# Optimization experiments

Hardware: AMD Instinct MI355X
Metric: run time of the kernel (lower is better)

The kernel has to match this reference:

```python
import jax, jax.numpy as jnp
import numpy as np

B, N, DIN, DOUT, T, R, H = 4, 384, 128, 128, 4, 4, 8
DK = DOUT // H
SQRT_DK = float(np.sqrt(DK))


def setup_inputs() -> dict:
    key = jax.random.key(0)
    k = jax.random.split(key, 12)
    node_features = jax.random.normal(k[0], (B, N, DIN), jnp.float32)
    nt = jax.random.uniform(k[1], (B, N, T), dtype=jnp.float32)
    node_types_soft = nt / nt.sum(-1, keepdims=True)  # soft type distribution
    adj_matrix_soft = jax.random.uniform(k[2], (B, N, N), dtype=jnp.float32)
    et = jax.random.uniform(k[3], (B, N, N, R), dtype=jnp.float32)
    edge_types_soft = et / et.sum(-1, keepdims=True)  # soft relation distribution
    s = 0.05  # ~xavier scale for 128x128
    return dict(
        node_features=node_features,
        node_types_soft=node_types_soft,
        adj_matrix_soft=adj_matrix_soft,
        edge_types_soft=edge_types_soft,
        kw=jax.random.normal(k[4], (T, DIN, DOUT), jnp.float32) * s,
        kb=jnp.zeros((T, DOUT), jnp.float32),
        qw=jax.random.normal(k[5], (T, DIN, DOUT), jnp.float32) * s,
        qb=jnp.zeros((T, DOUT), jnp.float32),
        vw=jax.random.normal(k[6], (T, DIN, DOUT), jnp.float32) * s,
        vb=jnp.zeros((T, DOUT), jnp.float32),
        aw=jax.random.normal(k[7], (T, DOUT, DOUT), jnp.float32) * s,
        ab=jnp.zeros((T, DOUT), jnp.float32),
        norm_w=jnp.ones((T, DOUT), jnp.float32),
        norm_b=jnp.zeros((T, DOUT), jnp.float32),
        rel_pri=jnp.ones((R, H), jnp.float32),
        rel_att=jax.random.normal(k[8], (R, H, DK, DK), jnp.float32) * 0.1,
        rel_msg=jax.random.normal(k[9], (R, H, DK, DK), jnp.float32) * 0.1,
        skip=jnp.ones((T,), jnp.float32),
    )


def _forward(node_features, node_types_soft, adj_matrix_soft, edge_types_soft,
             kw, kb, qw, qb, vw, vb, aw, ab, norm_w, norm_b,
             rel_pri, rel_att, rel_msg, skip):
    Bq, Nn, _ = node_features.shape
    nt = node_types_soft
    # per-type Q/K/V projections: [B,N,T,H,DK]
    q = (jnp.einsum('bni,tid->bntd', node_features, qw) + qb).reshape(Bq, Nn, T, H, DK)
    kk = (jnp.einsum('bni,tid->bntd', node_features, kw) + kb).reshape(Bq, Nn, T, H, DK)
    v = (jnp.einsum('bni,tid->bntd', node_features, vw) + vb).reshape(Bq, Nn, T, H, DK)

    res_att = jnp.zeros((Bq, Nn, Nn, H), node_features.dtype)
    res_msg = jnp.zeros((Bq, Nn, Nn, H, DK), node_features.dtype)
    for r in range(R):  # small fixed relation count; types/heads fully vectorized
        kr = jnp.einsum('bjshe,hed->bjshd', kk, rel_att[r])
        vr = jnp.einsum('bjshe,hed->bjshd', v, rel_msg[r])
        # fold target-type mask (applied at node j in the original) into k: [B,N,Tt,Ts,H,DK]
        krt = kr[:, :, None] * nt[:, :, :, None, None, None]
        # P[b,i,j,s,h] = sum_{t,d} q[b,i,t,h,d] * nt[b,j,t] * kr[b,j,s,h,d], scaled
        P = jnp.einsum('bithd,bjtshd->bijsh', q, krt) * (rel_pri[r] / SQRT_DK)
        mask = edge_types_soft[..., r] * adj_matrix_soft  # [B,N,N]
        res_att = res_att + jnp.einsum('bijsh,bis->bijh', P, nt) * mask[..., None]
        res_msg = res_msg + jnp.einsum('bijsh,bis,bjshd->bijhd', P, nt, vr) * mask[..., None, None]

    att_sum = res_att.sum(axis=1, keepdims=True)
    safe = jnp.where(att_sum > 1e-6, att_sum, jnp.ones_like(att_sum))
    attw = (res_att / safe) * (att_sum > 1e-6).astype(res_att.dtype)
    agg = jnp.einsum('btsh,btshd->bthd', attw, res_msg).reshape(Bq, Nn, DOUT)

    trans = jnp.einsum('bnd,tdo->bnto', agg, aw) + ab
    trans = jax.nn.gelu(trans, approximate=False)  # dropout = identity at eval
    alpha = jax.nn.sigmoid(skip)[None, None, :, None]
    # in_dim == out_dim -> identity skip projection
    res = trans * alpha + node_features[:, :, None, :] * (1.0 - alpha)
    mean = res.mean(-1, keepdims=True)
    var = res.var(-1, keepdims=True)
    res = (res - mean) / jnp.sqrt(var + 1e-5) * norm_w + norm_b
    return (res * nt[..., None]).sum(axis=2)  # [B,N,DOUT]


def reference(node_features, node_types_soft, adj_matrix_soft, edge_types_soft,
              kw, kb, qw, qb, vw, vb, aw, ab, norm_w, norm_b,
              rel_pri, rel_att, rel_msg, skip):
    return _forward(node_features, node_types_soft, adj_matrix_soft, edge_types_soft,
                    kw, kb, qw, qb, vw, vb, aw, ab, norm_w, norm_b,
                    rel_pri, rel_att, rel_msg, skip)
```

## Files before the change

### kernel.cpp

```cpp
#include <hip/hip_runtime.h>
#include <math.h>

#define Bq 4
#define Nn 384
#define NB 1536
#define TT 4
#define RR 4
#define HH 8
#define DKk 16
#define APART 12288

typedef __attribute__((ext_vector_type(8))) short short8;
typedef __attribute__((ext_vector_type(4))) float f32x4;

__device__ __forceinline__ unsigned short f2bf(float f) {
  unsigned u = __float_as_uint(f);
  u += 0x7FFFu + ((u >> 16) & 1u);
  return (unsigned short)(u >> 16);
}

__device__ __forceinline__ void ld16(const float* __restrict__ p, float* o) {
  const float4* p4 = reinterpret_cast<const float4*>(p);
  float4 a = p4[0], b = p4[1], c = p4[2], d = p4[3];
  o[0]=a.x; o[1]=a.y; o[2]=a.z; o[3]=a.w;
  o[4]=b.x; o[5]=b.y; o[6]=b.z; o[7]=b.w;
  o[8]=c.x; o[9]=c.y; o[10]=c.z; o[11]=c.w;
  o[12]=d.x; o[13]=d.y; o[14]=d.z; o[15]=d.w;
}

__device__ __forceinline__ void bar_lds() {
  asm volatile("s_waitcnt lgkmcnt(0)" ::: "memory");
  __builtin_amdgcn_s_barrier();
}


__global__ __launch_bounds__(256) void k1a_qkv(
    const float* __restrict__ nf,
    const float* __restrict__ qw, const float* __restrict__ qb,
    const float* __restrict__ kw, const float* __restrict__ kb,
    const float* __restrict__ vw, const float* __restrict__ vb,
    float* __restrict__ q_ws, float* __restrict__ kv_k, float* __restrict__ kv_v)
{
  __shared__ float A_s[32][72];
  __shared__ float W_s[32][132];
  int mt = blockIdx.x, t = blockIdx.y, z = blockIdx.z;
  const float* W    = (z == 0) ? qw : ((z == 1) ? kw : vw);
  const float* bias = (z == 0) ? qb : ((z == 1) ? kb : vb);
  int tid = threadIdx.x;
  int colq = (tid & 31)*4, n8 = (tid >> 5)*8;
  float acc[8][4];
#pragma unroll
  for (int u = 0; u < 8; ++u)
#pragma unroll
    for (int c = 0; c < 4; ++c) acc[u][c] = 0.f;

  for (int kc = 0; kc < 4; ++kc) {
    __syncthreads();
    {
      int kk = tid & 31, nb0 = tid >> 5;
#pragma unroll
      for (int u = 0; u < 8; ++u)
        A_s[kk][nb0 + u*8] = nf[(size_t)(mt*64 + nb0 + u*8)*128 + kc*32 + kk];
#pragma unroll
      for (int u = 0; u < 4; ++u) {
        int idx = u*256 + tid;
        int wk = idx >> 5, c4 = (idx & 31)*4;
        *(float4*)&W_s[wk][c4] = *(const float4*)&W[(size_t)(t*128 + kc*32 + wk)*128 + c4];
      }
    }
    __syncthreads();
#pragma unroll
    for (int k = 0; k < 32; ++k) {
      float4 w4 = *(float4*)&W_s[k][colq];
      float a0[8];
      *(float4*)&a0[0] = *(float4*)&A_s[k][n8];
      *(float4*)&a0[4] = *(float4*)&A_s[k][n8 + 4];
#pragma unroll
      for (int u = 0; u < 8; ++u) {
        acc[u][0] += a0[u]*w4.x; acc[u][1] += a0[u]*w4.y;
        acc[u][2] += a0[u]*w4.z; acc[u][3] += a0[u]*w4.w;
      }
    }
  }
  float4 bv = *(const float4*)&bias[t*128 + colq];
#pragma unroll
  for (int u = 0; u < 8; ++u) {
    int node = mt*64 + n8 + u;
    float4 o;
    o.x = acc[u][0] + bv.x; o.y = acc[u][1] + bv.y;
    o.z = acc[u][2] + bv.z; o.w = acc[u][3] + bv.w;
    if (z == 0) {
      int h = colq >> 4, d = colq & 15;
      *(float4*)&q_ws[((size_t)h*NB + node)*64 + t*16 + d] = o;
    } else {
      float* dst = (z == 1) ? kv_k : kv_v;
      *(float4*)&dst[(size_t)node*512 + t*128 + colq] = o;
    }
  }
}

__global__ __launch_bounds__(256) void k1b_rel(
    const float* __restrict__ kv_k, const float* __restrict__ kv_v,
    const float* __restrict__ rel_att, const float* __restrict__ rel_msg,
    float* __restrict__ kr_ws, float* __restrict__ vr_ws,
    float* __restrict__ agg)
{
  __shared__ float ra_s[4][16][16];
  __shared__ float rm_s[4][16][16];
  __shared__ float k_s[16][4][17];
  __shared__ float v_s[16][4][17];
  int nb = blockIdx.x, h = blockIdx.y;
  int n0 = nb*16;
  int tid = threadIdx.x;
  agg[(size_t)(n0 + (tid >> 4))*128 + h*16 + (tid & 15)] = 0.f;
#pragma unroll
  for (int u0 = 0; u0 < 4; ++u0) {
    int u = u0*256 + tid;
    int r = u >> 8, e = (u >> 4) & 15, d = u & 15;
    ra_s[r][e][d] = rel_att[((size_t)(r*8 + h)*16 + e)*16 + d];
    rm_s[r][e][d] = rel_msg[((size_t)(r*8 + h)*16 + e)*16 + d];
    int nl = u >> 6, s = (u >> 4) & 3, e2 = u & 15;
    k_s[nl][s][e2] = kv_k[(size_t)(n0 + nl)*512 + s*128 + h*16 + e2];
    v_s[nl][s][e2] = kv_v[(size_t)(n0 + nl)*512 + s*128 + h*16 + e2];
  }
  __syncthreads();
  int nl = tid >> 4, dq = tid & 15;
  size_t obase = ((size_t)h*NB + n0 + nl)*256;
#pragma unroll
  for (int r = 0; r < 4; ++r)
#pragma unroll
    for (int s = 0; s < 4; ++s) {
      float aK = 0.f, aV = 0.f;
#pragma unroll
      for (int e = 0; e < 16; ++e) {
        aK += k_s[nl][s][e] * ra_s[r][e][dq];
        aV += v_s[nl][s][e] * rm_s[r][e][dq];
      }
      kr_ws[obase + r*64 + s*16 + dq] = aK;
      vr_ws[obase + r*64 + s*16 + dq] = aV;
    }
}

__global__ __launch_bounds__(256,2) void k2_att(
    const float* __restrict__ nt, const float* __restrict__ adj,
    const float* __restrict__ ets, const float* __restrict__ rel_pri,
    const float* __restrict__ q_ws, const float* __restrict__ kr_ws,
    float* __restrict__ res_att, float* __restrict__ att_part)
{
  __shared__ float q_s[16*68];
  __shared__ float kr_s[32*260];
  __shared__ float ntj_s[32*4];
  int bx = blockIdx.x, h = blockIdx.y, b = blockIdx.z;
  int it = bx >> 1, jh = bx & 1;
  int i0 = it*16;
  int tid = threadIdx.x;
  int j_l = tid>>3, ig = (tid>>1)&3, dh = tid&1;
  {
    int i = tid>>4, f = (tid&15)*4;
    float4 qv = *(const float4*)&q_ws[((size_t)(h*NB) + b*Nn + i0 + i)*64 + f];
    *(float4*)&q_s[i*68 + f] = qv;
  }
  float ntiv[4][4];
#pragma unroll
  for (int il = 0; il < 4; ++il) {
    float4 v = *(const float4*)&nt[(size_t)(b*Nn + i0 + ig*4 + il)*TT];
    ntiv[il][0]=v.x; ntiv[il][1]=v.y; ntiv[il][2]=v.z; ntiv[il][3]=v.w;
  }
  float crr[4];
#pragma unroll
  for (int r = 0; r < 4; ++r) crr[r] = rel_pri[r*HH+h]*0.25f;

  for (int jc = jh*6; jc < jh*6 + 6; ++jc) {
    __syncthreads();
    {
      int js = tid>>3, gb = tid&7;
      const float* src = &kr_ws[((size_t)(h*NB) + b*Nn + jc*32 + js)*256];
      float* dst = &kr_s[js*260];
#pragma unroll
      for (int gl = 0; gl < 8; ++gl) {
        int g = gl*8 + gb;
        float4 v = *(const float4*)&src[g*4];
        int r = g>>4, s = (g>>2)&3, qd = g&3;
        int gd = (qd>>1)*32 + r*8 + s*2 + (qd&1);
        *(float4*)&dst[gd*4] = v;
      }
      if (tid < 128) ntj_s[tid] = nt[(size_t)(b*Nn + jc*32 + (tid>>2))*TT + (tid&3)];
    }
    __syncthreads();
    int j = jc*32 + j_l;
    float nt0 = ntj_s[j_l*4+0], nt1 = ntj_s[j_l*4+1];
    float nt2 = ntj_s[j_l*4+2], nt3 = ntj_s[j_l*4+3];
    float qn[4][8];
#pragma unroll
    for (int il = 0; il < 4; ++il) {
      const float* qb2 = &q_s[(ig*4 + il)*68 + dh*8];
      float4 a0 = *(const float4*)&qb2[0],  a1 = *(const float4*)&qb2[4];
      float4 b0 = *(const float4*)&qb2[16], b1 = *(const float4*)&qb2[20];
      float4 c0 = *(const float4*)&qb2[32], c1 = *(const float4*)&qb2[36];
      float4 d0v = *(const float4*)&qb2[48], d1v = *(const float4*)&qb2[52];
      qn[il][0] = a0.x*nt0 + b0.x*nt1 + c0.x*nt2 + d0v.x*nt3;
      qn[il][1] = a0.y*nt0 + b0.y*nt1 + c0.y*nt2 + d0v.y*nt3;
      qn[il][2] = a0.z*nt0 + b0.z*nt1 + c0.z*nt2 + d0v.z*nt3;
      qn[il][3] = a0.w*nt0 + b0.w*nt1 + c0.w*nt2 + d0v.w*nt3;
      qn[il][4] = a1.x*nt0 + b1.x*nt1 + c1.x*nt2 + d1v.x*nt3;
      qn[il][5] = a1.y*nt0 + b1.y*nt1 + c1.y*nt2 + d1v.y*nt3;
      qn[il][6] = a1.z*nt0 + b1.z*nt1 + c1.z*nt2 + d1v.z*nt3;
      qn[il][7] = a1.w*nt0 + b1.w*nt1 + c1.w*nt2 + d1v.w*nt3;
    }
    float mar[4][4];
#pragma unroll
    for (int il = 0; il < 4; ++il) {
      int i = i0 + ig*4 + il;
      float a = adj[((size_t)b*Nn + i)*Nn + j];
      float4 e4 = *(const float4*)&ets[(((size_t)b*Nn + i)*Nn + j)*RR];
      mar[il][0]=e4.x*a; mar[il][1]=e4.y*a; mar[il][2]=e4.z*a; mar[il][3]=e4.w*a;
    }
    float acc[4] = {0.f,0.f,0.f,0.f};
    const float* kbp = &kr_s[j_l*260 + dh*128];
#pragma unroll
    for (int r = 0; r < 4; ++r) {
      float mr0 = mar[0][r]*crr[r], mr1 = mar[1][r]*crr[r];
      float mr2 = mar[2][r]*crr[r], mr3 = mar[3][r]*crr[r];
#pragma unroll
      for (int s = 0; s < 4; ++s) {
        float kk[8];
        *(float4*)&kk[0] = *(const float4*)&kbp[r*32 + s*8];
        *(float4*)&kk[4] = *(const float4*)&kbp[r*32 + s*8 + 4];
        float d0=0,d1=0,d2=0,d3=0;
#pragma unroll
        for (int dp = 0; dp < 8; ++dp) {
          d0 += qn[0][dp]*kk[dp]; d1 += qn[1][dp]*kk[dp];
          d2 += qn[2][dp]*kk[dp]; d3 += qn[3][dp]*kk[dp];
        }
        acc[0] += mr0*ntiv[0][s]*d0;
        acc[1] += mr1*ntiv[1][s]*d1;
        acc[2] += mr2*ntiv[2][s]*d2;
        acc[3] += mr3*ntiv[3][s]*d3;
      }
    }
#pragma unroll
    for (int il = 0; il < 4; ++il)
      acc[il] += __shfl_xor(acc[il], 1);
    if (dh == 0) {
#pragma unroll
      for (int il = 0; il < 4; ++il)
        res_att[((size_t)(b*HH + h)*Nn + i0 + ig*4 + il)*Nn + j] = acc[il];
    }
    float v = acc[0] + acc[1] + acc[2] + acc[3];
    v += __shfl_xor(v, 2);
    v += __shfl_xor(v, 4);
    if ((tid & 7) == 0)
      att_part[(size_t)it*APART + (size_t)(b*HH + h)*Nn + j] = v;
  }
}

__global__ __launch_bounds__(256) void kc_agg(
    const float* __restrict__ nt, const float* __restrict__ adj,
    const float* __restrict__ ets, const float* __restrict__ rel_pri,
    const float* __restrict__ q_ws, const float* __restrict__ kr_ws,
    const float* __restrict__ vr_ws, const float* __restrict__ res_att,
    const float* __restrict__ att_part, float* __restrict__ agg)
{
  __shared__ __align__(16) unsigned short B_lds[4][64*72];
  __shared__ __align__(16) unsigned short vr_lds[64*72];
  __shared__ __align__(16) unsigned short Z_lds[4][16*72];
  __shared__ float ntj_s[256];
  __shared__ float inv_s[64];
  int it = blockIdx.x, jc = blockIdx.y, bh = blockIdx.z;
  int b = bh >> 3, h = bh & 7;
  int tid = threadIdx.x, w = tid >> 6, l = tid & 63;
  int j0 = jc*64;
  int ib = it*64 + w*16;
  int irow = ib + (l & 15);
  int iz = ib + ((l >> 4) << 2);
  int lq = (l >> 4) * 8;
  ntj_s[tid] = nt[(size_t)(b*Nn + j0 + (tid>>2))*4 + (tid&3)];
  if (tid < 64) {
    float s = 0.f;
#pragma unroll
    for (int p = 0; p < 24; ++p)
      s += att_part[(size_t)p*APART + (size_t)bh*Nn + j0 + tid];
    inv_s[tid] = (s > 1e-6f) ? 1.f/s : 0.f;
  }
  short8 af[4][2];
  {
    float q0[8], q1[8];
    const float* qp = &q_ws[((size_t)h*NB + b*Nn + irow)*64];
    *(float4*)&q0[0] = *(const float4*)&qp[lq];
    *(float4*)&q0[4] = *(const float4*)&qp[lq + 4];
    *(float4*)&q1[0] = *(const float4*)&qp[32 + lq];
    *(float4*)&q1[4] = *(const float4*)&qp[32 + lq + 4];
    float4 ntiv = *(const float4*)&nt[(size_t)(b*Nn + irow)*4];
    float nta[4] = {ntiv.x, ntiv.y, ntiv.z, ntiv.w};
#pragma unroll
    for (int s = 0; s < 4; ++s)
#pragma unroll
      for (int e = 0; e < 8; ++e) {
        af[s][0][e] = (short)f2bf(q0[e]*nta[s]);
        af[s][1][e] = (short)f2bf(q1[e]*nta[s]);
      }
  }
  float crv[4];
#pragma unroll
  for (int r = 0; r < 4; ++r) crv[r] = rel_pri[r*HH + h]*0.25f;
  float cw[4][4];
  int eo[4][4];
  const float* ebase = ets + (size_t)b*Nn*Nn*4;
#pragma unroll
  for (int tj = 0; tj < 4; ++tj) {
    int j = j0 + tj*16 + (l & 15);
#pragma unroll
    for (int p = 0; p < 4; ++p) {
      int i = iz + p;
      cw[tj][p] = res_att[((size_t)bh*Nn + i)*Nn + j]
                * adj[((size_t)b*Nn + i)*Nn + j];
      eo[tj][p] = (i*Nn + j)*4;
    }
  }
  f32x4 agg_acc = {0.f,0.f,0.f,0.f};
  int js = tid >> 2, ss = tid & 3;
  const float* krp = &kr_ws[((size_t)h*NB + b*Nn + j0 + js)*256 + ss*16];
  const float* vrp = &vr_ws[((size_t)h*NB + b*Nn + j0 + js)*256 + ss*16];
  float kvA[16], vvA[16];
  ld16(krp, kvA);
  ld16(vrp, vvA);
  bar_lds();
#pragma unroll
  for (int tj = 0; tj < 4; ++tj) {
    float inv = inv_s[tj*16 + (l & 15)];
#pragma unroll
    for (int p = 0; p < 4; ++p) cw[tj][p] *= inv;
  }

#pragma unroll
  for (int r = 0; r < 4; ++r) {
    if (r) bar_lds();
    {
      float crr = crv[r];
      float4 ntjv = *(const float4*)&ntj_s[js*4];
      float nta[4] = {ntjv.x*crr, ntjv.y*crr, ntjv.z*crr, ntjv.w*crr};
#pragma unroll
      for (int t = 0; t < 4; ++t) {
#pragma unroll
        for (int dq = 0; dq < 2; ++dq) {
          short8 v;
#pragma unroll
          for (int e = 0; e < 8; ++e) v[e] = (short)f2bf(kvA[dq*8 + e]*nta[t]);
          *(short8*)&B_lds[ss][js*72 + t*16 + dq*8] = v;
        }
      }
#pragma unroll
      for (int d = 0; d < 16; ++d)
        vr_lds[(ss*16 + d)*72 + js] = f2bf(vvA[d]);
    }
    float kvB[16], vvB[16];
    if (r < 3) {
      ld16(krp + (r+1)*64, kvB);
      ld16(vrp + (r+1)*64, vvB);
    }
    bar_lds();
    float coef[4][4];
#pragma unroll
    for (int tj = 0; tj < 4; ++tj)
#pragma unroll
      for (int p = 0; p < 4; ++p)
        coef[tj][p] = ebase[eo[tj][p] + r] * cw[tj][p];
#pragma unroll
    for (int s = 0; s < 4; ++s) {
      f32x4 wacc[4];
#pragma unroll
      for (int tj = 0; tj < 4; ++tj) wacc[tj] = (f32x4){0.f,0.f,0.f,0.f};
#pragma unroll
      for (int tj = 0; tj < 4; ++tj) {
        short8 b0 = *(const short8*)&B_lds[s][(tj*16 + (l & 15))*72 + lq];
        short8 b1 = *(const short8*)&B_lds[s][(tj*16 + (l & 15))*72 + 32 + lq];
        wacc[tj] = __builtin_amdgcn_mfma_f32_16x16x32_bf16(af[s][0], b0, wacc[tj], 0, 0, 0);
        wacc[tj] = __builtin_amdgcn_mfma_f32_16x16x32_bf16(af[s][1], b1, wacc[tj], 0, 0, 0);
      }
#pragma unroll
      for (int tj = 0; tj < 4; ++tj)
#pragma unroll
        for (int p = 0; p < 4; ++p)
          Z_lds[w][(((l >> 4)*4) + p)*72 + tj*16 + (l & 15)] = f2bf(wacc[tj][p]*coef[tj][p]);
#pragma unroll
      for (int kj = 0; kj < 2; ++kj) {
        short8 zf = *(const short8*)&Z_lds[w][(l & 15)*72 + kj*32 + lq];
        short8 vf = *(const short8*)&vr_lds[(s*16 + (l & 15))*72 + kj*32 + lq];
        agg_acc = __builtin_amdgcn_mfma_f32_16x16x32_bf16(zf, vf, agg_acc, 0, 0, 0);
      }
    }
    if (r < 3) {
#pragma unroll
      for (int e = 0; e < 16; ++e) { kvA[e] = kvB[e]; vvA[e] = vvB[e]; }
    }
  }
#pragma unroll
  for (int p = 0; p < 4; ++p)
    atomicAdd(&agg[((size_t)b*Nn + iz + p)*128 + h*16 + (l & 15)], agg_acc[p]);
}

__global__ __launch_bounds__(128) void k5_out(
    const float* __restrict__ agg_ws, const float* __restrict__ nf,
    const float* __restrict__ nt, const float* __restrict__ aw,
    const float* __restrict__ ab, const float* __restrict__ norm_w,
    const float* __restrict__ norm_b, const float* __restrict__ skip,
    float* __restrict__ out)
{
  __shared__ float agg_s[128];
  __shared__ float red[4];
  int n = blockIdx.x, b = blockIdx.y;
  int o = threadIdx.x;
  size_t node = (size_t)b*Nn + n;
  agg_s[o] = agg_ws[node*128 + o];
  __syncthreads();
  float nfo = nf[node*128 + o];
  float outacc = 0.f;
  for (int t = 0; t < TT; ++t) {
    float a = ab[t*128 + o];
    for (int dd = 0; dd < 128; ++dd) a += agg_s[dd] * aw[(size_t)(t*128 + dd)*128 + o];
    float g = 0.5f * a * (1.f + erff(a * 0.70710678118654752f));
    float alpha = 1.f / (1.f + expf(-skip[t]));
    float res = g*alpha + nfo*(1.f - alpha);
    float s1 = res, s2 = res*res;
#pragma unroll
    for (int m = 32; m >= 1; m >>= 1) { s1 += __shfl_xor(s1, m); s2 += __shfl_xor(s2, m); }
    int w = o >> 6;
    if ((o & 63) == 0) { red[w*2] = s1; red[w*2 + 1] = s2; }
    __syncthreads();
    float tot1 = red[0] + red[2], tot2 = red[1] + red[3];
    __syncthreads();
    float mean = tot1 * (1.f/128.f);
    float var  = tot2 * (1.f/128.f) - mean*mean;
    float nrm = (res - mean) * rsqrtf(var + 1e-5f) * norm_w[t*128 + o] + norm_b[t*128 + o];
    outacc += nrm * nt[node*TT + t];
  }
  out[node*128 + o] = outacc;
}

extern "C" void kernel_launch(void* const* d_in, const int* in_sizes, int n_in,
                              void* d_out, int out_size, void* d_ws, size_t ws_size,
                              hipStream_t stream) {
  const float* nf      = (const float*)d_in[0];
  const float* nts     = (const float*)d_in[1];
  const float* adj     = (const float*)d_in[2];
  const float* ets     = (const float*)d_in[3];
  const float* kw      = (const float*)d_in[4];
  const float* kb      = (const float*)d_in[5];
  const float* qw      = (const float*)d_in[6];
  const float* qb      = (const float*)d_in[7];
  const float* vw      = (const float*)d_in[8];
  const float* vb      = (const float*)d_in[9];
  const float* aw      = (const float*)d_in[10];
  const float* ab      = (const float*)d_in[11];
  const float* normw   = (const float*)d_in[12];
  const float* normb   = (const float*)d_in[13];
  const float* rel_pri = (const float*)d_in[14];
  const float* rel_att = (const float*)d_in[15];
  const float* rel_msg = (const float*)d_in[16];
  const float* skip    = (const float*)d_in[17];
  (void)in_sizes; (void)n_in; (void)out_size; (void)ws_size;

  float* ws = (float*)d_ws;
  float* q_ws    = ws;
  float* kr_ws   = q_ws + 786432;
  float* vr_ws   = kr_ws + 3145728;
  float* res_att = vr_ws + 3145728;
  float* att_part= res_att + 4718592;
  float* agg_ws  = att_part + 294912 + 12288;
  float* kv_k = res_att;
  float* kv_v = res_att + 786432;

  hipLaunchKernelGGL(k1a_qkv, dim3(24, 4, 3), dim3(256), 0, stream,
                     nf, qw, qb, kw, kb, vw, vb, q_ws, kv_k, kv_v);
  hipLaunchKernelGGL(k1b_rel, dim3(96, 8), dim3(256), 0, stream,
                     kv_k, kv_v, rel_att, rel_msg, kr_ws, vr_ws, agg_ws);
  hipLaunchKernelGGL(k2_att, dim3(48, 8, 4), dim3(256), 0, stream,
                     nts, adj, ets, rel_pri, q_ws, kr_ws, res_att, att_part);
  hipLaunchKernelGGL(kc_agg, dim3(6, 6, 32), dim3(256), 0, stream,
                     nts, adj, ets, rel_pri, q_ws, kr_ws, vr_ws, res_att, att_part, agg_ws);
  hipLaunchKernelGGL(k5_out, dim3(384, 4), dim3(128), 0, stream,
                     agg_ws, nf, nts, aw, ab, normw, normb, skip, (float*)d_out);
}
```

Measured before the change: 187.3 us.

## Parallelize output kernel over node types with atomics and simplify K shared layout

```diff
diff --git a/kernel.cpp b/kernel.cpp
--- a/kernel.cpp
+++ b/kernel.cpp
@@ -103,7 +103,7 @@
     const float* __restrict__ kv_k, const float* __restrict__ kv_v,
     const float* __restrict__ rel_att, const float* __restrict__ rel_msg,
     float* __restrict__ kr_ws, float* __restrict__ vr_ws,
-    float* __restrict__ agg)
+    float* __restrict__ agg, float* __restrict__ out)
 {
   __shared__ float ra_s[4][16][16];
   __shared__ float rm_s[4][16][16];
@@ -113,6 +113,7 @@
   int n0 = nb*16;
   int tid = threadIdx.x;
   agg[(size_t)(n0 + (tid >> 4))*128 + h*16 + (tid & 15)] = 0.f;
+  out[(size_t)(n0 + (tid >> 4))*128 + h*16 + (tid & 15)] = 0.f;
 #pragma unroll
   for (int u0 = 0; u0 < 4; ++u0) {
     int u = u0*256 + tid;
@@ -179,10 +180,7 @@
 #pragma unroll
       for (int gl = 0; gl < 8; ++gl) {
         int g = gl*8 + gb;
-        float4 v = *(const float4*)&src[g*4];
-        int r = g>>4, s = (g>>2)&3, qd = g&3;
-        int gd = (qd>>1)*32 + r*8 + s*2 + (qd&1);
-        *(float4*)&dst[gd*4] = v;
+        *(float4*)&dst[g*4] = *(const float4*)&src[g*4];
       }
       if (tid < 128) ntj_s[tid] = nt[(size_t)(b*Nn + jc*32 + (tid>>2))*TT + (tid&3)];
     }
@@ -216,7 +214,7 @@
       mar[il][0]=e4.x*a; mar[il][1]=e4.y*a; mar[il][2]=e4.z*a; mar[il][3]=e4.w*a;
     }
     float acc[4] = {0.f,0.f,0.f,0.f};
-    const float* kbp = &kr_s[j_l*260 + dh*128];
+    const float* kbp = &kr_s[j_l*260 + dh*8];
 #pragma unroll
     for (int r = 0; r < 4; ++r) {
       float mr0 = mar[0][r]*crr[r], mr1 = mar[1][r]*crr[r];
@@ -224,8 +222,8 @@
 #pragma unroll
       for (int s = 0; s < 4; ++s) {
         float kk[8];
-        *(float4*)&kk[0] = *(const float4*)&kbp[r*32 + s*8];
-        *(float4*)&kk[4] = *(const float4*)&kbp[r*32 + s*8 + 4];
+        *(float4*)&kk[0] = *(const float4*)&kbp[r*64 + s*16];
+        *(float4*)&kk[4] = *(const float4*)&kbp[r*64 + s*16 + 4];
         float d0=0,d1=0,d2=0,d3=0;
 #pragma unroll
         for (int dp = 0; dp < 8; ++dp) {
@@ -406,35 +404,51 @@
     const float* __restrict__ norm_b, const float* __restrict__ skip,
     float* __restrict__ out)
 {
-  __shared__ float agg_s[128];
-  __shared__ float red[4];
-  int n = blockIdx.x, b = blockIdx.y;
-  int o = threadIdx.x;
-  size_t node = (size_t)b*Nn + n;
-  agg_s[o] = agg_ws[node*128 + o];
+  __shared__ float agg_s[4][128];
+  int nq = blockIdx.x, t = blockIdx.y;
+  int tid = threadIdx.x;
+  int g = tid >> 5, o0 = (tid & 31)*4;
+  {
+    int nl = tid >> 5, c = (tid & 31)*4;
+    *(float4*)&agg_s[nl][c] = *(const float4*)&agg_ws[(size_t)(nq*4 + nl)*128 + c];
+  }
   __syncthreads();
-  float nfo = nf[node*128 + o];
-  float outacc = 0.f;
-  for (int t = 0; t < TT; ++t) {
-    float a = ab[t*128 + o];
-    for (int dd = 0; dd < 128; ++dd) a += agg_s[dd] * aw[(size_t)(t*128 + dd)*128 + o];
-    float g = 0.5f * a * (1.f + erff(a * 0.70710678118654752f));
-    float alpha = 1.f / (1.f + expf(-skip[t]));
-    float res = g*alpha + nfo*(1.f - alpha);
-    float s1 = res, s2 = res*res;
-#pragma unroll
-    for (int m = 32; m >= 1; m >>= 1) { s1 += __shfl_xor(s1, m); s2 += __shfl_xor(s2, m); }
-    int w = o >> 6;
-    if ((o & 63) == 0) { red[w*2] = s1; red[w*2 + 1] = s2; }
-    __syncthreads();
-    float tot1 = red[0] + red[2], tot2 = red[1] + red[3];
-    __syncthreads();
-    float mean = tot1 * (1.f/128.f);
-    float var  = tot2 * (1.f/128.f) - mean*mean;
-    float nrm = (res - mean) * rsqrtf(var + 1e-5f) * norm_w[t*128 + o] + norm_b[t*128 + o];
-    outacc += nrm * nt[node*TT + t];
-  }
-  out[node*128 + o] = outacc;
+  size_t node = (size_t)nq*4 + g;
+  float alpha = 1.f/(1.f + expf(-skip[t]));
+  float4 bv = *(const float4*)&ab[t*128 + o0];
+  float a0 = bv.x, a1 = bv.y, a2 = bv.z, a3 = bv.w;
+  const float* awt = aw + (size_t)t*128*128;
+  for (int dd = 0; dd < 128; ++dd) {
+    float av = agg_s[g][dd];
+    float4 wv = *(const float4*)&awt[dd*128 + o0];
+    a0 += av*wv.x; a1 += av*wv.y; a2 += av*wv.z; a3 += av*wv.w;
+  }
+  float4 nfv = *(const float4*)&nf[node*128 + o0];
+  float av4[4] = {a0, a1, a2, a3};
+  float nfa[4] = {nfv.x, nfv.y, nfv.z, nfv.w};
+  float res[4];
+#pragma unroll
+  for (int c = 0; c < 4; ++c) {
+    float gl = 0.5f*av4[c]*(1.f + erff(av4[c]*0.70710678118654752f));
+    res[c] = gl*alpha + nfa[c]*(1.f - alpha);
+  }
+  float s1 = res[0]+res[1]+res[2]+res[3];
+  float s2 = res[0]*res[0]+res[1]*res[1]+res[2]*res[2]+res[3]*res[3];
+#pragma unroll
+  for (int m = 16; m >= 1; m >>= 1) { s1 += __shfl_xor(s1, m); s2 += __shfl_xor(s2, m); }
+  float mean = s1*(1.f/128.f);
+  float var  = s2*(1.f/128.f) - mean*mean;
+  float rstd = rsqrtf(var + 1e-5f);
+  float ntv = nt[node*TT + t];
+  float4 nwv = *(const float4*)&norm_w[t*128 + o0];
+  float4 nbv = *(const float4*)&norm_b[t*128 + o0];
+  float nww[4] = {nwv.x, nwv.y, nwv.z, nwv.w};
+  float nbb[4] = {nbv.x, nbv.y, nbv.z, nbv.w};
+#pragma unroll
+  for (int c = 0; c < 4; ++c) {
+    float nrm = (res[c] - mean)*rstd*nww[c] + nbb[c];
+    atomicAdd(&out[node*128 + o0 + c], nrm*ntv);
+  }
 }
 
 extern "C" void kernel_launch(void* const* d_in, const int* in_sizes, int n_in,
@@ -473,7 +487,7 @@
   hipLaunchKernelGGL(k1a_qkv, dim3(24, 4, 3), dim3(256), 0, stream,
                      nf, qw, qb, kw, kb, vw, vb, q_ws, kv_k, kv_v);
   hipLaunchKernelGGL(k1b_rel, dim3(96, 8), dim3(256), 0, stream,
-                     kv_k, kv_v, rel_att, rel_msg, kr_ws, vr_ws, agg_ws);
+                     kv_k, kv_v, rel_att, rel_msg, kr_ws, vr_ws, agg_ws, (float*)d_out);
   hipLaunchKernelGGL(k2_att, dim3(48, 8, 4), dim3(256), 0, stream,
                      nts, adj, ets, rel_pri, q_ws, kr_ws, res_att, att_part);
   hipLaunchKernelGGL(kc_agg, dim3(6, 6, 32), dim3(256), 0, stream,
```

After: 184.0 us, median of 2. No clear change (-1.7%).
